# Kernel optimization log

Measured on AMD Instinct MI355X. Metric: run time of the kernel, lower is better.

Reference implementation:

```python
import jax, jax.numpy as jnp
import numpy as np
from jax.scipy.special import logsumexp

EPS = 0.05        # entropic regularization (blur^p)
N_ITERS = 20      # Sinkhorn iterations
N, M, D = 8192, 8192, 64


def setup_inputs() -> dict:
    key = jax.random.key(0)
    k1, k2, k3, k4 = jax.random.split(key, 4)
    return {
        "a": jax.random.uniform(k1, (N,), dtype=jnp.float32),
        "x": jax.random.normal(k2, (N, D), dtype=jnp.float32),
        "b": jax.random.uniform(k3, (M,), dtype=jnp.float32),
        "y": jax.random.normal(k4, (M, D), dtype=jnp.float32),
    }


def reference(a, x, b, y):
    eps = EPS
    # _normalize_weights: probability simplex
    a = a / jnp.sum(a)
    b = b / jnp.sum(b)
    loga = jnp.log(a)
    logb = jnp.log(b)
    # squared-Euclidean cost C_ij = ||x_i - y_j||^2, built via one GEMM (online kernel's math)
    x2 = jnp.sum(x * x, axis=1)            # [N]
    y2 = jnp.sum(y * y, axis=1)            # [M]
    C = x2[:, None] + y2[None, :] - 2.0 * (x @ y.T)   # [N, M]

    # log-domain Sinkhorn: f_i = -eps * LSE_j( log b_j + (g_j - C_ij)/eps )
    def softmin_rows(g_, C_, logw):   # reduce over columns j -> [N]
        return -eps * logsumexp(logw[None, :] + (g_[None, :] - C_) / eps, axis=1)

    def softmin_cols(f_, C_, logw):   # reduce over rows i -> [M]
        return -eps * logsumexp(logw[:, None] + (f_[:, None] - C_) / eps, axis=0)

    def body(i, fg):
        f_, g_ = fg
        f_ = softmin_rows(g_, C, logb)
        g_ = softmin_cols(f_, C, loga)
        return (f_, g_)

    f0 = jnp.zeros_like(a)
    g0 = jnp.zeros_like(b)
    f, g = jax.lax.fori_loop(0, N_ITERS, body, (f0, g0))

    # GeomLoss-style: one final symmetric update from detached potentials (Danskin)
    f_d = jax.lax.stop_gradient(f)
    g_d = jax.lax.stop_gradient(g)
    f_fin = softmin_rows(g_d, C, logb)
    g_fin = softmin_cols(f_d, C, loga)
    # OT_eps(a, b) = <a, f> + <b, g>
    return jnp.sum(a * f_fin) + jnp.sum(b * g_fin)
```

## Files before the change

kernel.cpp:

```cpp
#include <hip/hip_runtime.h>
#include <hip/hip_bf16.h>

#define EPS       0.05f
#define N_ITERS   20
#define NR        8192
#define DIM       64
#define LOG2E     1.4426950408889634f
#define LN2       0.6931471805599453f
#define S2        (2.0f * LOG2E / EPS)
#define EPSLN2    (EPS * LN2)
#define NEGINF    (-1e30f)
#define NSPLIT    16
#define PSZ       (NSPLIT * NR)

typedef __attribute__((ext_vector_type(8))) short short8;
typedef __attribute__((ext_vector_type(4))) float float4v;
typedef unsigned long long u64;

#define GLD_LDS16(src, dst)                                              \
    __builtin_amdgcn_global_load_lds(                                    \
        (const __attribute__((address_space(1))) void*)(src),            \
        (__attribute__((address_space(3))) void*)(dst), 16, 0, 0)

__device__ __forceinline__ float2 ld_f2a(const u64* p) {
    u64 v = __hip_atomic_load(p, __ATOMIC_RELAXED, __HIP_MEMORY_SCOPE_AGENT);
    union { u64 u; float2 f; } c; c.u = v; return c.f;
}
__device__ __forceinline__ void st_f2a(u64* p, float2 f) {
    union { u64 u; float2 f2; } c; c.f2 = f;
    __hip_atomic_store(p, c.u, __ATOMIC_RELAXED, __HIP_MEMORY_SCOPE_AGENT);
}

__device__ __forceinline__ float wave_reduce_sum(float v) {
    #pragma unroll
    for (int m = 1; m < 64; m <<= 1) v += __shfl_xor(v, m, 64);
    return v;
}

__device__ __forceinline__ float merge16_a(const u64* P, int i) {
    float2 p[NSPLIT];
    float M = NEGINF;
    #pragma unroll
    for (int k = 0; k < NSPLIT; k++) {
        p[k] = ld_f2a(P + k * NR + i);
        M = fmaxf(M, p[k].x);
    }
    float S = 0.f;
    #pragma unroll
    for (int k = 0; k < NSPLIT; k++)
        S += p[k].y * __builtin_amdgcn_exp2f(p[k].x - M);
    return M + __builtin_amdgcn_logf(S);
}

__device__ __forceinline__ void gsync_n(unsigned* bar, unsigned n) {
    __syncthreads();
    if (threadIdx.x == 0) {
        unsigned g = __hip_atomic_load(&bar[1], __ATOMIC_RELAXED,
                                       __HIP_MEMORY_SCOPE_AGENT);
        unsigned a = __hip_atomic_fetch_add(&bar[0], 1u, __ATOMIC_RELAXED,
                                            __HIP_MEMORY_SCOPE_AGENT);
        if (a == n - 1u) {
            __hip_atomic_store(&bar[0], 0u, __ATOMIC_RELAXED,
                               __HIP_MEMORY_SCOPE_AGENT);
            __hip_atomic_store(&bar[1], g + 1u, __ATOMIC_RELAXED,
                               __HIP_MEMORY_SCOPE_AGENT);
        } else {
            while (__hip_atomic_load(&bar[1], __ATOMIC_RELAXED,
                                     __HIP_MEMORY_SCOPE_AGENT) == g)
                __builtin_amdgcn_s_sleep(1);
        }
    }
    __syncthreads();
}

__global__ void sums_kernel(const float* __restrict__ a, const float* __restrict__ b,
                            float* __restrict__ sums, unsigned* __restrict__ barr) {
    __shared__ float red[32];
    int tid = threadIdx.x;
    if (tid < 1024) barr[tid] = 0u;
    float pa = 0.f, pb = 0.f;
    for (int i = tid; i < NR; i += blockDim.x) { pa += a[i]; pb += b[i]; }
    pa = wave_reduce_sum(pa);
    pb = wave_reduce_sum(pb);
    int wid = tid >> 6, ln = tid & 63;
    if (ln == 0) { red[wid] = pa; red[wid + 16] = pb; }
    __syncthreads();
    if (tid == 0) {
        float sa = 0.f, sb = 0.f;
        int nw = blockDim.x >> 6;
        for (int w = 0; w < nw; w++) { sa += red[w]; sb += red[w + 16]; }
        sums[0] = logf(sa); sums[1] = logf(sb); sums[2] = sa; sums[3] = sb;
    }
}

__global__ void prep_kernel(const float* __restrict__ x, const float* __restrict__ y,
                            const float* __restrict__ a, const float* __restrict__ b,
                            const float* __restrict__ sums,
                            short8* __restrict__ xs, short8* __restrict__ ys,
                            float* __restrict__ x2, float* __restrict__ y2,
                            float* __restrict__ la2, float* __restrict__ lb2,
                            float2* __restrict__ Pb1) {
    int gid = blockIdx.x * 256 + threadIdx.x;
    bool isx = gid < NR * 8;
    int cid = isx ? gid : gid - NR * 8;
    int row = cid >> 3;
    int c   = cid & 7;
    const float4* src = (const float4*)(isx ? x : y);
    float4 v0 = src[row * 16 + c * 2];
    float4 v1 = src[row * 16 + c * 2 + 1];

    const float sc = isx ? S2 : 1.0f;
    short8 st;
    st[0] = __bfloat16_as_short(__float2bfloat16(v0.x * sc));
    st[1] = __bfloat16_as_short(__float2bfloat16(v0.y * sc));
    st[2] = __bfloat16_as_short(__float2bfloat16(v0.z * sc));
    st[3] = __bfloat16_as_short(__float2bfloat16(v0.w * sc));
    st[4] = __bfloat16_as_short(__float2bfloat16(v1.x * sc));
    st[5] = __bfloat16_as_short(__float2bfloat16(v1.y * sc));
    st[6] = __bfloat16_as_short(__float2bfloat16(v1.z * sc));
    st[7] = __bfloat16_as_short(__float2bfloat16(v1.w * sc));

    int T = row >> 4, ln = row & 15, f = c >> 2, q = c & 3;
    (isx ? xs : ys)[T * 128 + f * 64 + q * 16 + ln] = st;

    float sq = v0.x*v0.x + v0.y*v0.y + v0.z*v0.z + v0.w*v0.w
             + v1.x*v1.x + v1.y*v1.y + v1.z*v1.z + v1.w*v1.w;
    #pragma unroll
    for (int m = 1; m < 8; m <<= 1) sq += __shfl_xor(sq, m, 64);

    if (c == 0) {
        if (isx) {
            x2[row] = sq;
            la2[row] = (logf(a[row]) - sums[0]) * LOG2E;
        } else {
            y2[row] = sq;
            lb2[row] = (logf(b[row]) - sums[1]) * LOG2E;
            Pb1[row] = make_float2(sq * (LOG2E / EPS), 1.0f);
            #pragma unroll
            for (int k = 1; k < NSPLIT; k++)
                Pb1[k * NR + row] = make_float2(NEGINF, 0.0f);
        }
    }
}

#define LSE4(acc, mm, ss)                                                \
    {                                                                    \
        float z0 = (acc)[0], z1 = (acc)[1];                              \
        float z2 = (acc)[2], z3 = (acc)[3];                              \
        float mn = fmaxf(fmaxf(fmaxf(z0, z1), fmaxf(z2, z3)), (mm));     \
        float e  = __builtin_amdgcn_exp2f((mm) - mn);                    \
        float p  = (__builtin_amdgcn_exp2f(z0 - mn)                      \
                  + __builtin_amdgcn_exp2f(z1 - mn))                     \
                 + (__builtin_amdgcn_exp2f(z2 - mn)                      \
                  + __builtin_amdgcn_exp2f(z3 - mn));                    \
        (ss) = fmaf((ss), e, p);                                         \
        (mm) = mn;                                                       \
    }

__device__ __forceinline__ void do_pass(
        const u64* Pin, const float* lw, u64* Pout,
        int colbase, int outidx, int roff, int coff,
        char* mlds, float* cbl, float2 (*comb)[3]) {
    const int tid = threadIdx.x;
    const int w   = tid >> 6, lane = tid & 63;
    const int quad = lane >> 4, ln = lane & 15;
    const int cst = w & 1, rq = w >> 1;

    if (tid < 512) {
        int jj = colbase + tid;
        cbl[tid] = lw[jj] - merge16_a(Pin, jj);
    }
    __syncthreads();

    short8 rf0[4], rf1[4];
    {
        const char* rw = &mlds[roff + rq * 8192];
        #pragma unroll
        for (int t = 0; t < 4; t++) {
            rf0[t] = *(const short8*)(rw + t * 2048 + lane * 16);
            rf1[t] = *(const short8*)(rw + t * 2048 + 1024 + lane * 16);
        }
    }

    float lm[4], ls[4];
    #pragma unroll
    for (int t = 0; t < 4; t++) { lm[t] = NEGINF; ls[t] = 0.f; }

    const char* cw = &mlds[coff + cst * 32768];
    const float* cbw = cbl + cst * 256;
    #pragma unroll 4
    for (int u = 0; u < 16; u++) {
        short8 ya0 = *(const short8*)(cw + u * 2048 + lane * 16);
        short8 ya1 = *(const short8*)(cw + u * 2048 + 1024 + lane * 16);
        float4v cin = *(const float4v*)(cbw + u * 16 + quad * 4);
        #pragma unroll
        for (int tt = 0; tt < 4; tt++) {
            float4v acc = __builtin_amdgcn_mfma_f32_16x16x32_bf16(ya0, rf0[tt], cin, 0, 0, 0);
            acc = __builtin_amdgcn_mfma_f32_16x16x32_bf16(ya1, rf1[tt], acc, 0, 0, 0);
            LSE4(acc, lm[tt], ls[tt]);
        }
    }

    #pragma unroll
    for (int mask = 16; mask < 64; mask <<= 1) {
        #pragma unroll
        for (int t = 0; t < 4; t++) {
            float mo = __shfl_xor(lm[t], mask, 64);
            float so = __shfl_xor(ls[t], mask, 64);
            float M  = fmaxf(lm[t], mo);
            ls[t] = ls[t] * __builtin_amdgcn_exp2f(lm[t] - M)
                  + so    * __builtin_amdgcn_exp2f(mo    - M);
            lm[t] = M;
        }
    }

    __syncthreads();
    if (lane < 16) {
        #pragma unroll
        for (int t = 0; t < 4; t++)
            comb[rq * 64 + t * 16 + ln][cst] = make_float2(lm[t], ls[t]);
    }
    __syncthreads();

    if (tid < 512) {
        float2 c0 = comb[tid][0], c1 = comb[tid][1];
        float M = fmaxf(c0.x, c1.x);
        float S = c0.y * __builtin_amdgcn_exp2f(c0.x - M)
                + c1.y * __builtin_amdgcn_exp2f(c1.x - M);
        st_f2a(Pout + outidx + tid, make_float2(M, S));
    }
}

__global__ __launch_bounds__(1024, 4) void sink_kernel(
        const short8* __restrict__ xs, const short8* __restrict__ ys,
        const float* __restrict__ la2, const float* __restrict__ lb2,
        u64* P,
        const float* __restrict__ a, const float* __restrict__ b,
        const float* __restrict__ x2, const float* __restrict__ y2,
        u64* red2, const float* __restrict__ sums,
        unsigned* barr, float* out) {
    __shared__ __attribute__((aligned(16))) char mlds[131072];
    __shared__ __attribute__((aligned(16))) float cbl[512];
    __shared__ float2 comb[512][3];

    const int tid = threadIdx.x;
    const int bi  = blockIdx.x;
    const int ib  = bi >> 4, jb = bi & 15;

    u64* Pf[2] = { P,           P + PSZ };
    u64* Pb[2] = { P + 2 * PSZ, P + 3 * PSZ };
    u64* Pff   = P;
    u64* Pgf   = P + 2 * PSZ;
    unsigned* rbar = barr + ib * 32;
    unsigned* cbar = barr + (16 + jb) * 32;

    const int w = tid >> 6;
    const char* xsrc = (const char*)xs + (size_t)(ib * 512) * 128;
    const char* ysrc = (const char*)ys + (size_t)(jb * 512) * 128;
    #pragma unroll
    for (int r = 0; r < 4; r++) {
        GLD_LDS16(xsrc + r * 16384 + tid * 16, &mlds[r * 16384 + w * 1024]);
        GLD_LDS16(ysrc + r * 16384 + tid * 16, &mlds[65536 + r * 16384 + w * 1024]);
    }

    for (int t = 0; t < N_ITERS; t++) {
        const int par = t & 1;
        do_pass(Pb[par ^ 1], lb2, Pf[par],
                512 * jb, jb * NR + 512 * ib, 0, 65536, mlds, cbl, comb);
        gsync_n(rbar, 16);
        do_pass(Pf[par], la2, Pb[par],
                512 * ib, ib * NR + 512 * jb, 65536, 0, mlds, cbl, comb);
        gsync_n(cbar, 16);
    }

    do_pass(Pb[1], lb2, Pff, 512 * jb, jb * NR + 512 * ib, 0, 65536,
            mlds, cbl, comb);
    do_pass(Pf[1], la2, Pgf, 512 * ib, ib * NR + 512 * jb, 65536, 0,
            mlds, cbl, comb);
    gsync_n(rbar, 16);
    gsync_n(cbar, 16);

    if (bi < 64 && tid < 256) {
        int r = bi * 128 + (tid & 127);
        bool gsd = tid >= 128;
        float L  = merge16_a(gsd ? Pgf : Pff, r);
        float sq = gsd ? y2[r] : x2[r];
        float wv = gsd ? b[r]  : a[r];
        float v  = wv * (sq - EPSLN2 * L);
        v = wave_reduce_sum(v);
        if ((tid & 63) == 0) cbl[tid >> 6] = v;
    }
    __syncthreads();
    if (bi < 64 && tid == 0)
        st_f2a(red2 + bi, make_float2(cbl[0] + cbl[1], cbl[2] + cbl[3]));
    gsync_n(rbar, 16);
    gsync_n(cbar, 16);

    if (bi == 0 && tid < 64) {
        float2 v = ld_f2a(red2 + tid);
        float da = wave_reduce_sum(v.x);
        float db = wave_reduce_sum(v.y);
        if (tid == 0) out[0] = da / sums[2] + db / sums[3];
    }
}

extern "C" void kernel_launch(void* const* d_in, const int* in_sizes, int n_in,
                              void* d_out, int out_size, void* d_ws, size_t ws_size,
                              hipStream_t stream) {
    const float* a = (const float*)d_in[0];
    const float* x = (const float*)d_in[1];
    const float* b = (const float*)d_in[2];
    const float* y = (const float*)d_in[3];

    char* ws = (char*)d_ws;
    short8* xs = (short8*)ws;
    short8* ys = (short8*)(ws + (1 << 20));
    float* fp  = (float*)(ws + (2 << 20));
    float* x2  = fp;
    float* y2  = fp + NR;
    float* la2 = fp + 2 * NR;
    float* lb2 = fp + 3 * NR;
    u64* P     = (u64*)(fp + 4 * NR);
    u64* red2  = P + 4 * PSZ;
    float* sums  = (float*)(red2 + 64);
    unsigned* barr = (unsigned*)(ws + (7 << 20));
    float* outp  = (float*)d_out;

    sums_kernel<<<1, 1024, 0, stream>>>(a, b, sums, barr);
    prep_kernel<<<(2 * NR * 8) / 256, 256, 0, stream>>>(x, y, a, b, sums,
                                                        xs, ys,
                                                        x2, y2, la2, lb2,
                                                        (float2*)(P + 3 * PSZ));

    void* args[] = { (void*)&xs, (void*)&ys, (void*)&la2, (void*)&lb2,
                     (void*)&P, (void*)&a, (void*)&b, (void*)&x2, (void*)&y2,
                     (void*)&red2, (void*)&sums, (void*)&barr, (void*)&outp };
    hipLaunchCooperativeKernel((void*)sink_kernel, dim3(256), dim3(1024),
                               args, 0, stream);
}
```

Before: 872.5 us.

## Split Sinkhorn work over 512 smaller blocks and restage column tiles at barriers

Adds a second cooperative kernel that launches 512 blocks of 512 threads. Each block owns 256 rows and keeps a 64KB LDS tile of columns that it re-stages around every group barrier, while row fragments are loaded straight from global memory. The goal is to fill all CUs with two blocks each and to overlap the column staging with barrier waiting. The price is twice as many partial results, 32-block barriers, and restaging the column tile twice per iteration. An occupancy query decides at runtime which kernel to launch, keeping the old kernel as a fallback.

```diff
diff --git a/kernel.cpp b/kernel.cpp
--- a/kernel.cpp
+++ b/kernel.cpp
@@ -55,6 +55,37 @@
 __device__ __forceinline__ void gsync_n(unsigned* bar, unsigned n) {
     __syncthreads();
     if (threadIdx.x == 0) {
+        unsigned g = __hip_atomic_load(&bar[1], __ATOMIC_RELAXED,
+                                       __HIP_MEMORY_SCOPE_AGENT);
+        unsigned a = __hip_atomic_fetch_add(&bar[0], 1u, __ATOMIC_RELAXED,
+                                            __HIP_MEMORY_SCOPE_AGENT);
+        if (a == n - 1u) {
+            __hip_atomic_store(&bar[0], 0u, __ATOMIC_RELAXED,
+                               __HIP_MEMORY_SCOPE_AGENT);
+            __hip_atomic_store(&bar[1], g + 1u, __ATOMIC_RELAXED,
+                               __HIP_MEMORY_SCOPE_AGENT);
+        } else {
+            while (__hip_atomic_load(&bar[1], __ATOMIC_RELAXED,
+                                     __HIP_MEMORY_SCOPE_AGENT) == g)
+                __builtin_amdgcn_s_sleep(1);
+        }
+    }
+    __syncthreads();
+}
+
+__device__ __forceinline__ void stage_cols(const char* src, char* clds,
+                                           int tid, int w) {
+    #pragma unroll
+    for (int k = 0; k < 8; k++)
+        GLD_LDS16(src + k * 8192 + (size_t)tid * 16, &clds[k * 8192 + w * 1024]);
+}
+
+__device__ __forceinline__ void gsync_stage(unsigned* bar, unsigned n,
+                                            const char* src, char* clds,
+                                            int tid, int w) {
+    __syncthreads();
+    if (src) stage_cols(src, clds, tid, w);
+    if (tid == 0) {
         unsigned g = __hip_atomic_load(&bar[1], __ATOMIC_RELAXED,
                                        __HIP_MEMORY_SCOPE_AGENT);
         unsigned a = __hip_atomic_fetch_add(&bar[0], 1u, __ATOMIC_RELAXED,
@@ -157,7 +188,7 @@
         (mm) = mn;                                                       \
     }
 
-__device__ __forceinline__ void do_pass(
+__device__ __forceinline__ void do_pass_b(
         const u64* Pin, const float* lw, u64* Pout,
         int colbase, int outidx, int roff, int coff,
         char* mlds, float* cbl, float2 (*comb)[3]) {
@@ -231,11 +262,10 @@
     }
 }
 
-__global__ __launch_bounds__(1024, 4) void sink_kernel(
+__global__ __launch_bounds__(1024, 4) void sink_kernel1(
         const short8* __restrict__ xs, const short8* __restrict__ ys,
         const float* __restrict__ la2, const float* __restrict__ lb2,
-        u64* P,
-        const float* __restrict__ a, const float* __restrict__ b,
+        u64* P, const float* __restrict__ a, const float* __restrict__ b,
         const float* __restrict__ x2, const float* __restrict__ y2,
         u64* red2, const float* __restrict__ sums,
         unsigned* barr, float* out) {
@@ -265,18 +295,18 @@
 
     for (int t = 0; t < N_ITERS; t++) {
         const int par = t & 1;
-        do_pass(Pb[par ^ 1], lb2, Pf[par],
-                512 * jb, jb * NR + 512 * ib, 0, 65536, mlds, cbl, comb);
+        do_pass_b(Pb[par ^ 1], lb2, Pf[par],
+                  512 * jb, jb * NR + 512 * ib, 0, 65536, mlds, cbl, comb);
         gsync_n(rbar, 16);
-        do_pass(Pf[par], la2, Pb[par],
-                512 * ib, ib * NR + 512 * jb, 65536, 0, mlds, cbl, comb);
+        do_pass_b(Pf[par], la2, Pb[par],
+                  512 * ib, ib * NR + 512 * jb, 65536, 0, mlds, cbl, comb);
         gsync_n(cbar, 16);
     }
 
-    do_pass(Pb[1], lb2, Pff, 512 * jb, jb * NR + 512 * ib, 0, 65536,
-            mlds, cbl, comb);
-    do_pass(Pf[1], la2, Pgf, 512 * ib, ib * NR + 512 * jb, 65536, 0,
-            mlds, cbl, comb);
+    do_pass_b(Pb[1], lb2, Pff, 512 * jb, jb * NR + 512 * ib, 0, 65536,
+              mlds, cbl, comb);
+    do_pass_b(Pf[1], la2, Pgf, 512 * ib, ib * NR + 512 * jb, 65536, 0,
+              mlds, cbl, comb);
     gsync_n(rbar, 16);
     gsync_n(cbar, 16);
 
@@ -295,6 +325,136 @@
         st_f2a(red2 + bi, make_float2(cbl[0] + cbl[1], cbl[2] + cbl[3]));
     gsync_n(rbar, 16);
     gsync_n(cbar, 16);
+
+    if (bi == 0 && tid < 64) {
+        float2 v = ld_f2a(red2 + tid);
+        float da = wave_reduce_sum(v.x);
+        float db = wave_reduce_sum(v.y);
+        if (tid == 0) out[0] = da / sums[2] + db / sums[3];
+    }
+}
+
+__device__ __forceinline__ void do_pass_s(
+        const u64* Pin, const float* lw, u64* Pout,
+        int colbase, const char* rowsrc, char* clds, float* cbl) {
+    const int tid = threadIdx.x;
+    const int w = tid >> 6, lane = tid & 63;
+    const int quad = lane >> 4, ln = lane & 15;
+
+    short8 rf0[2], rf1[2];
+    const char* rsrc = rowsrc + (size_t)(w * 2) * 2048 + (size_t)lane * 16;
+    #pragma unroll
+    for (int t = 0; t < 2; t++) {
+        rf0[t] = *(const short8*)(rsrc + t * 2048);
+        rf1[t] = *(const short8*)(rsrc + t * 2048 + 1024);
+    }
+
+    {
+        int j = colbase + tid;
+        cbl[tid] = lw[j] - merge16_a(Pin, j);
+    }
+    __syncthreads();
+
+    float lm[2] = { NEGINF, NEGINF }, ls[2] = { 0.f, 0.f };
+    #pragma unroll 4
+    for (int u = 0; u < 32; u++) {
+        short8 ya0 = *(const short8*)(clds + u * 2048 + lane * 16);
+        short8 ya1 = *(const short8*)(clds + u * 2048 + 1024 + lane * 16);
+        float4v cin = *(const float4v*)(cbl + u * 16 + quad * 4);
+        #pragma unroll
+        for (int tt = 0; tt < 2; tt++) {
+            float4v acc = __builtin_amdgcn_mfma_f32_16x16x32_bf16(ya0, rf0[tt], cin, 0, 0, 0);
+            acc = __builtin_amdgcn_mfma_f32_16x16x32_bf16(ya1, rf1[tt], acc, 0, 0, 0);
+            LSE4(acc, lm[tt], ls[tt]);
+        }
+    }
+
+    #pragma unroll
+    for (int mask = 16; mask < 64; mask <<= 1) {
+        #pragma unroll
+        for (int t = 0; t < 2; t++) {
+            float mo = __shfl_xor(lm[t], mask, 64);
+            float so = __shfl_xor(ls[t], mask, 64);
+            float M  = fmaxf(lm[t], mo);
+            ls[t] = ls[t] * __builtin_amdgcn_exp2f(lm[t] - M)
+                  + so    * __builtin_amdgcn_exp2f(mo    - M);
+            lm[t] = M;
+        }
+    }
+    if (lane < 16) {
+        #pragma unroll
+        for (int t = 0; t < 2; t++)
+            st_f2a(Pout + w * 32 + t * 16 + ln, make_float2(lm[t], ls[t]));
+    }
+}
+
+__global__ __launch_bounds__(512, 4) void sink_kernel2(
+        const short8* __restrict__ xs, const short8* __restrict__ ys,
+        const float* __restrict__ la2, const float* __restrict__ lb2,
+        u64* P, const float* __restrict__ a, const float* __restrict__ b,
+        const float* __restrict__ x2, const float* __restrict__ y2,
+        u64* red2, const float* __restrict__ sums,
+        unsigned* barr, float* out) {
+    __shared__ __attribute__((aligned(16))) char clds[65536];
+    __shared__ __attribute__((aligned(16))) float cbl[512];
+
+    const int tid = threadIdx.x;
+    const int bi  = blockIdx.x;
+    const int rb  = bi >> 4;
+    const int jb  = bi & 15;
+    const int w   = tid >> 6;
+    const int rgY = 2 * jb + (rb & 1);
+
+    u64* Pf[2] = { P,           P + PSZ };
+    u64* Pb[2] = { P + 2 * PSZ, P + 3 * PSZ };
+    u64* Pff   = P;
+    u64* Pgf   = P + 2 * PSZ;
+    unsigned* rbar = barr + (rb >> 1) * 32;
+    unsigned* cbar = barr + (16 + jb) * 32;
+
+    const char* xs_c = (const char*)xs;
+    const char* ys_c = (const char*)ys;
+    const char* fcol = ys_c + (size_t)jb * 65536;
+    const char* gcol = xs_c + (size_t)(rb >> 1) * 65536;
+    const char* frow = xs_c + (size_t)rb * 32768;
+    const char* grow = ys_c + (size_t)rgY * 32768;
+
+    stage_cols(fcol, clds, tid, w);
+
+    for (int t = 0; t < N_ITERS; t++) {
+        const int par = t & 1;
+        do_pass_s(Pb[par ^ 1], lb2, Pf[par] + jb * NR + 256 * rb,
+                  512 * jb, frow, clds, cbl);
+        gsync_stage(rbar, 32, gcol, clds, tid, w);
+        do_pass_s(Pf[par], la2, Pb[par] + (rb >> 1) * NR + 256 * rgY,
+                  512 * (rb >> 1), grow, clds, cbl);
+        gsync_stage(cbar, 32, fcol, clds, tid, w);
+    }
+
+    do_pass_s(Pb[1], lb2, Pff + jb * NR + 256 * rb, 512 * jb, frow, clds, cbl);
+    __syncthreads();
+    stage_cols(gcol, clds, tid, w);
+    do_pass_s(Pf[1], la2, Pgf + (rb >> 1) * NR + 256 * rgY,
+              512 * (rb >> 1), grow, clds, cbl);
+
+    gsync_stage(rbar, 32, nullptr, clds, tid, w);
+    gsync_stage(cbar, 32, nullptr, clds, tid, w);
+
+    if (bi < 64 && tid < 256) {
+        int r = bi * 128 + (tid & 127);
+        bool gsd = tid >= 128;
+        float L  = merge16_a(gsd ? Pgf : Pff, r);
+        float sq = gsd ? y2[r] : x2[r];
+        float wv = gsd ? b[r]  : a[r];
+        float v  = wv * (sq - EPSLN2 * L);
+        v = wave_reduce_sum(v);
+        if ((tid & 63) == 0) cbl[tid >> 6] = v;
+    }
+    __syncthreads();
+    if (bi < 64 && tid == 0)
+        st_f2a(red2 + bi, make_float2(cbl[0] + cbl[1], cbl[2] + cbl[3]));
+    gsync_stage(rbar, 32, nullptr, clds, tid, w);
+    gsync_stage(cbar, 32, nullptr, clds, tid, w);
 
     if (bi == 0 && tid < 64) {
         float2 v = ld_f2a(red2 + tid);
@@ -335,6 +495,15 @@
     void* args[] = { (void*)&xs, (void*)&ys, (void*)&la2, (void*)&lb2,
                      (void*)&P, (void*)&a, (void*)&b, (void*)&x2, (void*)&y2,
                      (void*)&red2, (void*)&sums, (void*)&barr, (void*)&outp };
-    hipLaunchCooperativeKernel((void*)sink_kernel, dim3(256), dim3(1024),
-                               args, 0, stream);
-}
+
+    int nb2 = 0;
+    hipError_t qe = hipOccupancyMaxActiveBlocksPerMultiprocessor(
+        &nb2, (const void*)sink_kernel2, 512, 0);
+    if (qe == hipSuccess && nb2 >= 2) {
+        hipLaunchCooperativeKernel((void*)sink_kernel2, dim3(512), dim3(512),
+                                   args, 0, stream);
+    } else {
+        hipLaunchCooperativeKernel((void*)sink_kernel1, dim3(256), dim3(1024),
+                                   args, 0, stream);
+    }
+}
```

New measurement: 871.8 us. Within noise of the previous version (-0.1%).
